# Kernel tuning notes

Measured on AMD Instinct MI355X. Metric: run time of the kernel, lower is better.

Reference implementation:

```python
import jax, jax.numpy as jnp
import numpy as np

T = 35            # cfg.VOXEL_POINT_COUNT
D, H, W = 10, 400, 352  # cfg.INPUT_DEPTH/HEIGHT/WIDTH
EPS = 1e-5


def _vfe(x, mask, w, b, gamma, beta):
    # x: [K, T, Cin]; mask: [K, T, 1]
    h = jax.nn.relu(jnp.einsum('ktc,cu->ktu', x, w) + b)        # [K, T, U]
    mean = jnp.mean(h, axis=(0, 1))
    var = jnp.var(h, axis=(0, 1))
    h = (h - mean) * jax.lax.rsqrt(var + EPS) * gamma + beta    # batch-stat BN
    agg = jnp.max(h, axis=1, keepdims=True)                     # [K, 1, U]
    cat = jnp.concatenate([h, jnp.broadcast_to(agg, h.shape)], axis=-1)  # [K, T, 2U]
    return cat * mask


def setup_inputs() -> dict:
    key = jax.random.key(0)
    ks = jax.random.split(key, 12)
    K = 40000
    feature = jax.random.normal(ks[0], (K, T, 7), dtype=jnp.float32)
    # zero out ~half the points so the nonzero mask is meaningful
    keep = jax.random.bernoulli(ks[1], 0.5, (K, T, 1)).astype(jnp.float32)
    feature = feature * keep
    bidx = jax.random.randint(ks[2], (K, 1), 0, 2)
    didx = jax.random.randint(ks[3], (K, 1), 0, D)
    hidx = jax.random.randint(ks[4], (K, 1), 0, H)
    widx = jax.random.randint(ks[5], (K, 1), 0, W)
    coordinate = jnp.concatenate([bidx, didx, hidx, widx], axis=1).astype(jnp.int32)
    s = 0.1
    return {
        'feature': feature,
        'w1': jax.random.normal(ks[6], (7, 16), dtype=jnp.float32) * s,
        'b1': jnp.zeros((16,), dtype=jnp.float32),
        'gamma1': jnp.ones((16,), dtype=jnp.float32),
        'beta1': jnp.zeros((16,), dtype=jnp.float32),
        'w2': jax.random.normal(ks[7], (32, 32), dtype=jnp.float32) * s,
        'b2': jnp.zeros((32,), dtype=jnp.float32),
        'gamma2': jnp.ones((32,), dtype=jnp.float32),
        'beta2': jnp.zeros((32,), dtype=jnp.float32),
        'coordinate': coordinate,
        'batch_size': 2,
    }


def reference(feature, w1, b1, gamma1, beta1, w2, b2, gamma2, beta2, coordinate, batch_size):
    # mask: voxel point is valid if any channel nonzero (max over channels != 0)
    mask = (jnp.max(feature, axis=2, keepdims=True) != 0).astype(feature.dtype)  # [K, T, 1]
    x = _vfe(feature, mask, w1, b1, gamma1, beta1)   # [K, T, 32]
    x = _vfe(x, mask, w2, b2, gamma2, beta2)         # [K, T, 64]
    voxelwise = jnp.max(x, axis=1)                   # [K, 64]
    out = jnp.zeros((batch_size, D, H, W, 64), dtype=voxelwise.dtype)
    out = out.at[coordinate[:, 0], coordinate[:, 1], coordinate[:, 2], coordinate[:, 3]].add(voxelwise)
    return out
```

## Files before the change

kernel.cpp:

```cpp
#include <hip/hip_runtime.h>
#include <math.h>

#define TT 35
#define DD 10
#define HD 400
#define WD 352
#define CIN 7
#define U1 16
#define U2 32
#define EPSV 1e-5f

#define WS_SUM1 256
#define WS_SSQ1 768
#define WS_SUM2 1280
#define WS_SSQ2 1792
#define NC1 32
#define NC2 16
#define WS_ZERO_FLOATS 2304
#define WS_SUM_OFF 4096

typedef __bf16 bf16x8 __attribute__((ext_vector_type(8)));
typedef float f32x4 __attribute__((ext_vector_type(4)));

__device__ inline unsigned short f2bf(float x) {
  unsigned u = __builtin_bit_cast(unsigned, x);
  unsigned r = (u + 0x7fff + ((u >> 16) & 1)) >> 16;
  return (unsigned short)r;
}

__global__ __launch_bounds__(256) void k_stats1(
    const float* __restrict__ feat, const float* __restrict__ w1,
    const float* __restrict__ b1, float* __restrict__ ws, int P) {
  __shared__ float s_w1[CIN * U1];
  __shared__ float s_b1[U1];
  __shared__ float s_red[4][2 * U1];

  int tid = threadIdx.x;
  if (tid < CIN * U1) s_w1[tid] = w1[tid];
  if (tid < U1) s_b1[tid] = b1[tid];
  __syncthreads();

  float sum[U1], ssq[U1];
#pragma unroll
  for (int u = 0; u < U1; ++u) { sum[u] = 0.f; ssq[u] = 0.f; }

  int stride = gridDim.x * blockDim.x;
  for (int p = blockIdx.x * blockDim.x + tid; p < P; p += stride) {
    const float* f = feat + (size_t)p * CIN;
    float x[CIN];
#pragma unroll
    for (int c = 0; c < CIN; ++c) x[c] = f[c];
#pragma unroll
    for (int u = 0; u < U1; ++u) {
      float acc = s_b1[u];
#pragma unroll
      for (int c = 0; c < CIN; ++c) acc += x[c] * s_w1[c * U1 + u];
      float h = fmaxf(acc, 0.f);
      sum[u] += h;
      ssq[u] += h * h;
    }
  }

  int lane = tid & 63, wv = tid >> 6;
#pragma unroll
  for (int u = 0; u < U1; ++u) {
    float s = sum[u], q = ssq[u];
    for (int off = 32; off; off >>= 1) {
      s += __shfl_down(s, off);
      q += __shfl_down(q, off);
    }
    if (lane == 0) { s_red[wv][u] = s; s_red[wv][U1 + u] = q; }
  }
  __syncthreads();
  if (tid < 2 * U1) {
    float tot = s_red[0][tid] + s_red[1][tid] + s_red[2][tid] + s_red[3][tid];
    int copy = blockIdx.x & (NC1 - 1);
    int u = tid & (U1 - 1);
    int base = (tid < U1) ? WS_SUM1 : WS_SSQ1;
    atomicAdd(&ws[base + copy * U1 + u], tot);
  }
}

__global__ __launch_bounds__(256) void k_vfe2(
    const float* __restrict__ feat, const float* __restrict__ w1,
    const float* __restrict__ b1, const float* __restrict__ g1,
    const float* __restrict__ be1, const float* __restrict__ w2,
    const float* __restrict__ b2, float* __restrict__ ws,
    float* __restrict__ sumg, float* __restrict__ cntg, int K, float invN) {
  __shared__ unsigned short s_w2b[32 * 40];
  __shared__ unsigned short s_catb[4][48][32];
  __shared__ float s_mk[4][40];
  __shared__ float s_red[4][64];

  int tid = threadIdx.x;
  int lane = tid & 63, wv = tid >> 6;
  int g = lane >> 4, u = lane & 15;
  int v = blockIdx.x * 4 + wv;
  bool active = (v < K);

  for (int i = tid; i < 32 * 32; i += 256) {
    int n = i >> 5, cp = i & 31;
    int c = (cp & 1) ? (16 + (cp >> 1)) : (cp >> 1);
    s_w2b[n * 40 + cp] = f2bf(w2[c * 32 + n]);
  }
  {
    unsigned* z = (unsigned*)s_catb;
    for (int i = tid; i < 4 * 13 * 16; i += 256) {
      int w = i / 208, rem = i % 208;
      int row = 35 + (rem >> 4), k = rem & 15;
      z[(w * 48 + row) * 16 + k] = 0u;
    }
  }

  float s1 = 0.f, q1 = 0.f;
#pragma unroll
  for (int c = 0; c < NC1; ++c) {
    s1 += ws[WS_SUM1 + c * U1 + u];
    q1 += ws[WS_SSQ1 + c * U1 + u];
  }
  float mean1 = s1 * invN;
  float var1 = q1 * invN - mean1 * mean1;
  float A1 = g1[u] / sqrtf(var1 + EPSV);
  float B1 = be1[u] - mean1 * A1;

  float w1r[CIN];
#pragma unroll
  for (int c = 0; c < CIN; ++c) w1r[c] = w1[c * U1 + u];
  float b1u = b1[u];

  float h1n[9], mkv[9];
  float aggl = -INFINITY;
  float cntl = 0.f;
  const float* fv = feat + (size_t)v * (TT * CIN);
#pragma unroll
  for (int j = 0; j < 9; ++j) {
    int t = g + 4 * j;
    h1n[j] = -INFINITY;
    mkv[j] = 0.f;
    if (active && t < TT) {
      const float* fr = fv + t * CIN;
      float x0 = fr[0], x1 = fr[1], x2 = fr[2], x3 = fr[3];
      float x4 = fr[4], x5 = fr[5], x6 = fr[6];
      float m = fmaxf(fmaxf(fmaxf(x0, x1), fmaxf(x2, x3)),
                      fmaxf(fmaxf(x4, x5), x6));
      float mk = (m != 0.f) ? 1.f : 0.f;
      float acc = b1u + x0 * w1r[0] + x1 * w1r[1] + x2 * w1r[2] +
                  x3 * w1r[3] + x4 * w1r[4] + x5 * w1r[5] + x6 * w1r[6];
      float h = fmaxf(acc, 0.f);
      h1n[j] = A1 * h + B1;
      mkv[j] = mk;
      cntl += mk;
      if (u == 0) s_mk[wv][t] = mk;
      aggl = fmaxf(aggl, h1n[j]);
    }
  }
  aggl = fmaxf(aggl, __shfl_xor(aggl, 16));
  aggl = fmaxf(aggl, __shfl_xor(aggl, 32));
  cntl += __shfl_xor(cntl, 16);
  cntl += __shfl_xor(cntl, 32);
  if (active && lane == 0) cntg[v] = cntl;

#pragma unroll
  for (int j = 0; j < 9; ++j) {
    int t = g + 4 * j;
    if (active && t < TT) {
      unsigned pk = (unsigned)f2bf(h1n[j] * mkv[j]) |
                    ((unsigned)f2bf(aggl * mkv[j]) << 16);
      *(unsigned*)&s_catb[wv][t][2 * u] = pk;
    }
  }
  __syncthreads();

  f32x4 acc[2][3];
#pragma unroll
  for (int nt = 0; nt < 2; ++nt)
#pragma unroll
    for (int mt = 0; mt < 3; ++mt) acc[nt][mt] = (f32x4)(0.f);

  bf16x8 bfr[2];
#pragma unroll
  for (int nt = 0; nt < 2; ++nt) {
    uint4 raw = *(const uint4*)&s_w2b[(nt * 16 + u) * 40 + g * 8];
    bfr[nt] = __builtin_bit_cast(bf16x8, raw);
  }
#pragma unroll
  for (int mt = 0; mt < 3; ++mt) {
    uint4 raw = *(const uint4*)&s_catb[wv][mt * 16 + u][g * 8];
    bf16x8 afr = __builtin_bit_cast(bf16x8, raw);
#pragma unroll
    for (int nt = 0; nt < 2; ++nt)
      acc[nt][mt] =
          __builtin_amdgcn_mfma_f32_16x16x32_bf16(afr, bfr[nt], acc[nt][mt], 0, 0, 0);
  }

  float b2c[2] = {b2[u], b2[16 + u]};
  float sum[2] = {0.f, 0.f}, ssq[2] = {0.f, 0.f};
  float maxm[2] = {-INFINITY, -INFINITY}, minm[2] = {INFINITY, INFINITY};
  float maxa[2] = {-INFINITY, -INFINITY}, mina[2] = {INFINITY, INFINITY};
#pragma unroll
  for (int nt = 0; nt < 2; ++nt) {
#pragma unroll
    for (int mt = 0; mt < 3; ++mt) {
#pragma unroll
      for (int r = 0; r < 4; ++r) {
        int row = mt * 16 + g * 4 + r;
        if (row < TT) {
          float h = fmaxf(acc[nt][mt][r] + b2c[nt], 0.f);
          sum[nt] += h;
          ssq[nt] += h * h;
          maxa[nt] = fmaxf(maxa[nt], h);
          mina[nt] = fminf(mina[nt], h);
          float mk = s_mk[wv][row];
          if (mk != 0.f) {
            maxm[nt] = fmaxf(maxm[nt], h);
            minm[nt] = fminf(minm[nt], h);
          }
        }
      }
    }
  }

#pragma unroll
  for (int nt = 0; nt < 2; ++nt) {
    sum[nt] += __shfl_xor(sum[nt], 16);
    sum[nt] += __shfl_xor(sum[nt], 32);
    ssq[nt] += __shfl_xor(ssq[nt], 16);
    ssq[nt] += __shfl_xor(ssq[nt], 32);
    maxa[nt] = fmaxf(maxa[nt], __shfl_xor(maxa[nt], 16));
    maxa[nt] = fmaxf(maxa[nt], __shfl_xor(maxa[nt], 32));
    mina[nt] = fminf(mina[nt], __shfl_xor(mina[nt], 16));
    mina[nt] = fminf(mina[nt], __shfl_xor(mina[nt], 32));
    maxm[nt] = fmaxf(maxm[nt], __shfl_xor(maxm[nt], 16));
    maxm[nt] = fmaxf(maxm[nt], __shfl_xor(maxm[nt], 32));
    minm[nt] = fminf(minm[nt], __shfl_xor(minm[nt], 16));
    minm[nt] = fminf(minm[nt], __shfl_xor(minm[nt], 32));
  }
  if (active && g == 0) {
#pragma unroll
    for (int nt = 0; nt < 2; ++nt) {
      float4 sm = make_float4(maxm[nt], minm[nt], maxa[nt], mina[nt]);
      *(float4*)&sumg[(size_t)v * 128 + (nt * 16 + u) * 4] = sm;
    }
  }

  float contrib = 0.f;
  if (active) {
    contrib = (g == 0) ? sum[0] : (g == 1) ? sum[1] : (g == 2) ? ssq[0] : ssq[1];
  }
  s_red[wv][(g & 1) * 16 + u + (g >> 1) * 32] = contrib;
  __syncthreads();
  if (tid < 64) {
    float tot = s_red[0][tid] + s_red[1][tid] + s_red[2][tid] + s_red[3][tid];
    int copy = blockIdx.x & (NC2 - 1);
    int ch = tid & 31;
    int base = (tid < 32) ? WS_SUM2 : WS_SSQ2;
    atomicAdd(&ws[base + copy * U2 + ch], tot);
  }
}

__global__ __launch_bounds__(256) void k_final(
    const float* __restrict__ sumg, const float* __restrict__ cntg,
    const float* __restrict__ ws, const float* __restrict__ g2,
    const float* __restrict__ be2, const int* __restrict__ coord,
    float* __restrict__ out, int K, float invN) {
  int tid = threadIdx.x;
  int v = blockIdx.x * 8 + (tid >> 5);
  int ch = tid & 31;
  if (v >= K) return;

  float s = 0.f, q = 0.f;
#pragma unroll
  for (int c = 0; c < NC2; ++c) {
    s += ws[WS_SUM2 + c * U2 + ch];
    q += ws[WS_SSQ2 + c * U2 + ch];
  }
  float mean = s * invN;
  float var = q * invN - mean * mean;
  float A2 = g2[ch] / sqrtf(var + EPSV);
  float B2 = be2[ch] - mean * A2;

  float4 sm = *(const float4*)&sumg[(size_t)v * 128 + ch * 4];
  float cnt = cntg[v];

  float hm = (A2 >= 0.f) ? (A2 * sm.x + B2) : (A2 * sm.y + B2);
  float ag = (A2 >= 0.f) ? (A2 * sm.z + B2) : (A2 * sm.w + B2);
  float voxr = (cnt < 0.5f) ? 0.f : ((cnt > TT - 0.5f) ? hm : fmaxf(hm, 0.f));
  float voxa = (cnt < 0.5f) ? 0.f : ((cnt > TT - 0.5f) ? ag : fmaxf(ag, 0.f));

  const int4 cd = *(const int4*)&coord[4 * v];
  long base = ((((long)cd.x * DD + cd.y) * HD + cd.z) * WD + cd.w) * 64;
  atomicAdd(&out[base + ch], voxr);
  atomicAdd(&out[base + 32 + ch], voxa);
}

extern "C" void kernel_launch(void* const* d_in, const int* in_sizes, int n_in,
                              void* d_out, int out_size, void* d_ws,
                              size_t ws_size, hipStream_t stream) {
  const float* feat = (const float*)d_in[0];
  const float* w1 = (const float*)d_in[1];
  const float* b1 = (const float*)d_in[2];
  const float* g1 = (const float*)d_in[3];
  const float* be1 = (const float*)d_in[4];
  const float* w2 = (const float*)d_in[5];
  const float* b2 = (const float*)d_in[6];
  const float* g2 = (const float*)d_in[7];
  const float* be2 = (const float*)d_in[8];
  const int* coord = (const int*)d_in[9];
  float* out = (float*)d_out;
  float* ws = (float*)d_ws;

  int K = in_sizes[0] / (TT * CIN);
  int P = K * TT;
  float invN = 1.0f / (float)P;

  float* sumg = ws + WS_SUM_OFF;
  float* cntg = sumg + (size_t)K * 128;

  (void)hipMemsetAsync(d_out, 0, (size_t)out_size * sizeof(float), stream);
  (void)hipMemsetAsync(d_ws, 0, WS_ZERO_FLOATS * sizeof(float), stream);

  k_stats1<<<512, 256, 0, stream>>>(feat, w1, b1, ws, P);

  int vb = (K + 3) / 4;
  k_vfe2<<<vb, 256, 0, stream>>>(feat, w1, b1, g1, be1, w2, b2, ws, sumg, cntg,
                                 K, invN);
  k_final<<<(K + 7) / 8, 256, 0, stream>>>(sumg, cntg, ws, g2, be2, coord, out,
                                           K, invN);
}
```

Baseline: 834.2 us.

## Loop k_vfe2 blocks over voxel groups and compute BN coefficients once per block

k_vfe2 now runs a grid-stride loop in which each block handles four groups of four voxels. The bf16 W2 staging, zero padding, layer-1 BN statistics reduction and weight register loads are therefore done once per block and reused across groups. The layer-1 and layer-2 BN scale/shift reductions are computed once per block in shared memory, instead of every thread reading all the partial-sum copies. k_final gets the same treatment, and k_stats1 launches four times as many blocks. This trims redundant global reads and setup work, at the cost of fewer k_vfe2 blocks and an extra barrier per loop iteration. The large output memset and the scatter atomics are untouched.

```diff
diff --git a/kernel.cpp b/kernel.cpp
--- a/kernel.cpp
+++ b/kernel.cpp
@@ -86,17 +86,17 @@
     const float* __restrict__ b1, const float* __restrict__ g1,
     const float* __restrict__ be1, const float* __restrict__ w2,
     const float* __restrict__ b2, float* __restrict__ ws,
-    float* __restrict__ sumg, float* __restrict__ cntg, int K, float invN) {
+    float* __restrict__ sumg, float* __restrict__ cntg, int K, float invN,
+    int G) {
   __shared__ unsigned short s_w2b[32 * 40];
   __shared__ unsigned short s_catb[4][48][32];
   __shared__ float s_mk[4][40];
   __shared__ float s_red[4][64];
+  __shared__ float s_A1[U1], s_B1[U1];
 
   int tid = threadIdx.x;
   int lane = tid & 63, wv = tid >> 6;
   int g = lane >> 4, u = lane & 15;
-  int v = blockIdx.x * 4 + wv;
-  bool active = (v < K);
 
   for (int i = tid; i < 32 * 32; i += 256) {
     int n = i >> 5, cp = i & 31;
@@ -111,150 +111,162 @@
       z[(w * 48 + row) * 16 + k] = 0u;
     }
   }
-
-  float s1 = 0.f, q1 = 0.f;
-#pragma unroll
-  for (int c = 0; c < NC1; ++c) {
-    s1 += ws[WS_SUM1 + c * U1 + u];
-    q1 += ws[WS_SSQ1 + c * U1 + u];
-  }
-  float mean1 = s1 * invN;
-  float var1 = q1 * invN - mean1 * mean1;
-  float A1 = g1[u] / sqrtf(var1 + EPSV);
-  float B1 = be1[u] - mean1 * A1;
-
+  if (tid < 32) {
+    int ch = tid & 15;
+    int base = (tid < 16) ? WS_SUM1 : WS_SSQ1;
+    float acc = 0.f;
+#pragma unroll
+    for (int c = 0; c < NC1; ++c) acc += ws[base + c * U1 + ch];
+    s_red[0][tid] = acc;
+  }
+  __syncthreads();
+  if (tid < 16) {
+    float s = s_red[0][tid], q = s_red[0][16 + tid];
+    float mean = s * invN;
+    float var = q * invN - mean * mean;
+    float A = g1[tid] / sqrtf(var + EPSV);
+    s_A1[tid] = A;
+    s_B1[tid] = be1[tid] - mean * A;
+  }
+  __syncthreads();
+
+  float A1 = s_A1[u], B1 = s_B1[u];
   float w1r[CIN];
 #pragma unroll
   for (int c = 0; c < CIN; ++c) w1r[c] = w1[c * U1 + u];
   float b1u = b1[u];
-
-  float h1n[9], mkv[9];
-  float aggl = -INFINITY;
-  float cntl = 0.f;
-  const float* fv = feat + (size_t)v * (TT * CIN);
-#pragma unroll
-  for (int j = 0; j < 9; ++j) {
-    int t = g + 4 * j;
-    h1n[j] = -INFINITY;
-    mkv[j] = 0.f;
-    if (active && t < TT) {
-      const float* fr = fv + t * CIN;
-      float x0 = fr[0], x1 = fr[1], x2 = fr[2], x3 = fr[3];
-      float x4 = fr[4], x5 = fr[5], x6 = fr[6];
-      float m = fmaxf(fmaxf(fmaxf(x0, x1), fmaxf(x2, x3)),
-                      fmaxf(fmaxf(x4, x5), x6));
-      float mk = (m != 0.f) ? 1.f : 0.f;
-      float acc = b1u + x0 * w1r[0] + x1 * w1r[1] + x2 * w1r[2] +
-                  x3 * w1r[3] + x4 * w1r[4] + x5 * w1r[5] + x6 * w1r[6];
-      float h = fmaxf(acc, 0.f);
-      h1n[j] = A1 * h + B1;
-      mkv[j] = mk;
-      cntl += mk;
-      if (u == 0) s_mk[wv][t] = mk;
-      aggl = fmaxf(aggl, h1n[j]);
-    }
-  }
-  aggl = fmaxf(aggl, __shfl_xor(aggl, 16));
-  aggl = fmaxf(aggl, __shfl_xor(aggl, 32));
-  cntl += __shfl_xor(cntl, 16);
-  cntl += __shfl_xor(cntl, 32);
-  if (active && lane == 0) cntg[v] = cntl;
-
-#pragma unroll
-  for (int j = 0; j < 9; ++j) {
-    int t = g + 4 * j;
-    if (active && t < TT) {
-      unsigned pk = (unsigned)f2bf(h1n[j] * mkv[j]) |
-                    ((unsigned)f2bf(aggl * mkv[j]) << 16);
-      *(unsigned*)&s_catb[wv][t][2 * u] = pk;
-    }
-  }
-  __syncthreads();
-
-  f32x4 acc[2][3];
-#pragma unroll
-  for (int nt = 0; nt < 2; ++nt)
-#pragma unroll
-    for (int mt = 0; mt < 3; ++mt) acc[nt][mt] = (f32x4)(0.f);
-
+  float b2c[2] = {b2[u], b2[16 + u]};
   bf16x8 bfr[2];
 #pragma unroll
   for (int nt = 0; nt < 2; ++nt) {
     uint4 raw = *(const uint4*)&s_w2b[(nt * 16 + u) * 40 + g * 8];
     bfr[nt] = __builtin_bit_cast(bf16x8, raw);
   }
-#pragma unroll
-  for (int mt = 0; mt < 3; ++mt) {
-    uint4 raw = *(const uint4*)&s_catb[wv][mt * 16 + u][g * 8];
-    bf16x8 afr = __builtin_bit_cast(bf16x8, raw);
+
+  for (int grp = blockIdx.x; grp < G; grp += gridDim.x) {
+    __syncthreads();
+    int v = grp * 4 + wv;
+    bool active = (v < K);
+
+    float h1n[9], mkv[9];
+    float aggl = -INFINITY;
+    float cntl = 0.f;
+    const float* fv = feat + (size_t)v * (TT * CIN);
+#pragma unroll
+    for (int j = 0; j < 9; ++j) {
+      int t = g + 4 * j;
+      h1n[j] = -INFINITY;
+      mkv[j] = 0.f;
+      if (active && t < TT) {
+        const float* fr = fv + t * CIN;
+        float x0 = fr[0], x1 = fr[1], x2 = fr[2], x3 = fr[3];
+        float x4 = fr[4], x5 = fr[5], x6 = fr[6];
+        float m = fmaxf(fmaxf(fmaxf(x0, x1), fmaxf(x2, x3)),
+                        fmaxf(fmaxf(x4, x5), x6));
+        float mk = (m != 0.f) ? 1.f : 0.f;
+        float acc = b1u + x0 * w1r[0] + x1 * w1r[1] + x2 * w1r[2] +
+                    x3 * w1r[3] + x4 * w1r[4] + x5 * w1r[5] + x6 * w1r[6];
+        float h = fmaxf(acc, 0.f);
+        h1n[j] = A1 * h + B1;
+        mkv[j] = mk;
+        cntl += mk;
+        if (u == 0) s_mk[wv][t] = mk;
+        aggl = fmaxf(aggl, h1n[j]);
+      }
+    }
+    aggl = fmaxf(aggl, __shfl_xor(aggl, 16));
+    aggl = fmaxf(aggl, __shfl_xor(aggl, 32));
+    cntl += __shfl_xor(cntl, 16);
+    cntl += __shfl_xor(cntl, 32);
+    if (active && lane == 0) cntg[v] = cntl;
+
+#pragma unroll
+    for (int j = 0; j < 9; ++j) {
+      int t = g + 4 * j;
+      if (active && t < TT) {
+        unsigned pk = (unsigned)f2bf(h1n[j] * mkv[j]) |
+                      ((unsigned)f2bf(aggl * mkv[j]) << 16);
+        *(unsigned*)&s_catb[wv][t][2 * u] = pk;
+      }
+    }
+
+    f32x4 acc[2][3];
 #pragma unroll
     for (int nt = 0; nt < 2; ++nt)
-      acc[nt][mt] =
-          __builtin_amdgcn_mfma_f32_16x16x32_bf16(afr, bfr[nt], acc[nt][mt], 0, 0, 0);
-  }
-
-  float b2c[2] = {b2[u], b2[16 + u]};
-  float sum[2] = {0.f, 0.f}, ssq[2] = {0.f, 0.f};
-  float maxm[2] = {-INFINITY, -INFINITY}, minm[2] = {INFINITY, INFINITY};
-  float maxa[2] = {-INFINITY, -INFINITY}, mina[2] = {INFINITY, INFINITY};
-#pragma unroll
-  for (int nt = 0; nt < 2; ++nt) {
+#pragma unroll
+      for (int mt = 0; mt < 3; ++mt) acc[nt][mt] = (f32x4)(0.f);
 #pragma unroll
     for (int mt = 0; mt < 3; ++mt) {
-#pragma unroll
-      for (int r = 0; r < 4; ++r) {
-        int row = mt * 16 + g * 4 + r;
-        if (row < TT) {
-          float h = fmaxf(acc[nt][mt][r] + b2c[nt], 0.f);
-          sum[nt] += h;
-          ssq[nt] += h * h;
-          maxa[nt] = fmaxf(maxa[nt], h);
-          mina[nt] = fminf(mina[nt], h);
-          float mk = s_mk[wv][row];
-          if (mk != 0.f) {
-            maxm[nt] = fmaxf(maxm[nt], h);
-            minm[nt] = fminf(minm[nt], h);
+      uint4 raw = *(const uint4*)&s_catb[wv][mt * 16 + u][g * 8];
+      bf16x8 afr = __builtin_bit_cast(bf16x8, raw);
+#pragma unroll
+      for (int nt = 0; nt < 2; ++nt)
+        acc[nt][mt] = __builtin_amdgcn_mfma_f32_16x16x32_bf16(afr, bfr[nt],
+                                                              acc[nt][mt], 0, 0, 0);
+    }
+
+    float sum[2] = {0.f, 0.f}, ssq[2] = {0.f, 0.f};
+    float maxm[2] = {-INFINITY, -INFINITY}, minm[2] = {INFINITY, INFINITY};
+    float maxa[2] = {-INFINITY, -INFINITY}, mina[2] = {INFINITY, INFINITY};
+#pragma unroll
+    for (int nt = 0; nt < 2; ++nt) {
+#pragma unroll
+      for (int mt = 0; mt < 3; ++mt) {
+#pragma unroll
+        for (int r = 0; r < 4; ++r) {
+          int row = mt * 16 + g * 4 + r;
+          if (row < TT) {
+            float h = fmaxf(acc[nt][mt][r] + b2c[nt], 0.f);
+            sum[nt] += h;
+            ssq[nt] += h * h;
+            maxa[nt] = fmaxf(maxa[nt], h);
+            mina[nt] = fminf(mina[nt], h);
+            float mk = s_mk[wv][row];
+            if (mk != 0.f) {
+              maxm[nt] = fmaxf(maxm[nt], h);
+              minm[nt] = fminf(minm[nt], h);
+            }
           }
         }
       }
     }
-  }
-
-#pragma unroll
-  for (int nt = 0; nt < 2; ++nt) {
-    sum[nt] += __shfl_xor(sum[nt], 16);
-    sum[nt] += __shfl_xor(sum[nt], 32);
-    ssq[nt] += __shfl_xor(ssq[nt], 16);
-    ssq[nt] += __shfl_xor(ssq[nt], 32);
-    maxa[nt] = fmaxf(maxa[nt], __shfl_xor(maxa[nt], 16));
-    maxa[nt] = fmaxf(maxa[nt], __shfl_xor(maxa[nt], 32));
-    mina[nt] = fminf(mina[nt], __shfl_xor(mina[nt], 16));
-    mina[nt] = fminf(mina[nt], __shfl_xor(mina[nt], 32));
-    maxm[nt] = fmaxf(maxm[nt], __shfl_xor(maxm[nt], 16));
-    maxm[nt] = fmaxf(maxm[nt], __shfl_xor(maxm[nt], 32));
-    minm[nt] = fminf(minm[nt], __shfl_xor(minm[nt], 16));
-    minm[nt] = fminf(minm[nt], __shfl_xor(minm[nt], 32));
-  }
-  if (active && g == 0) {
+
 #pragma unroll
     for (int nt = 0; nt < 2; ++nt) {
-      float4 sm = make_float4(maxm[nt], minm[nt], maxa[nt], mina[nt]);
-      *(float4*)&sumg[(size_t)v * 128 + (nt * 16 + u) * 4] = sm;
-    }
-  }
-
-  float contrib = 0.f;
-  if (active) {
-    contrib = (g == 0) ? sum[0] : (g == 1) ? sum[1] : (g == 2) ? ssq[0] : ssq[1];
-  }
-  s_red[wv][(g & 1) * 16 + u + (g >> 1) * 32] = contrib;
-  __syncthreads();
-  if (tid < 64) {
-    float tot = s_red[0][tid] + s_red[1][tid] + s_red[2][tid] + s_red[3][tid];
-    int copy = blockIdx.x & (NC2 - 1);
-    int ch = tid & 31;
-    int base = (tid < 32) ? WS_SUM2 : WS_SSQ2;
-    atomicAdd(&ws[base + copy * U2 + ch], tot);
+      sum[nt] += __shfl_xor(sum[nt], 16);
+      sum[nt] += __shfl_xor(sum[nt], 32);
+      ssq[nt] += __shfl_xor(ssq[nt], 16);
+      ssq[nt] += __shfl_xor(ssq[nt], 32);
+      maxa[nt] = fmaxf(maxa[nt], __shfl_xor(maxa[nt], 16));
+      maxa[nt] = fmaxf(maxa[nt], __shfl_xor(maxa[nt], 32));
+      mina[nt] = fminf(mina[nt], __shfl_xor(mina[nt], 16));
+      mina[nt] = fminf(mina[nt], __shfl_xor(mina[nt], 32));
+      maxm[nt] = fmaxf(maxm[nt], __shfl_xor(maxm[nt], 16));
+      maxm[nt] = fmaxf(maxm[nt], __shfl_xor(maxm[nt], 32));
+      minm[nt] = fminf(minm[nt], __shfl_xor(minm[nt], 16));
+      minm[nt] = fminf(minm[nt], __shfl_xor(minm[nt], 32));
+    }
+    if (active && g == 0) {
+#pragma unroll
+      for (int nt = 0; nt < 2; ++nt) {
+        float4 sm = make_float4(maxm[nt], minm[nt], maxa[nt], mina[nt]);
+        *(float4*)&sumg[(size_t)v * 128 + (nt * 16 + u) * 4] = sm;
+      }
+    }
+
+    float contrib = 0.f;
+    if (active) {
+      contrib = (g == 0) ? sum[0] : (g == 1) ? sum[1] : (g == 2) ? ssq[0] : ssq[1];
+    }
+    s_red[wv][(g & 1) * 16 + u + (g >> 1) * 32] = contrib;
+    __syncthreads();
+    if (tid < 64) {
+      float tot = s_red[0][tid] + s_red[1][tid] + s_red[2][tid] + s_red[3][tid];
+      int copy = blockIdx.x & (NC2 - 1);
+      int ch = tid & 31;
+      int base = (tid < 32) ? WS_SUM2 : WS_SSQ2;
+      atomicAdd(&ws[base + copy * U2 + ch], tot);
+    }
   }
 }
 
@@ -263,34 +275,45 @@
     const float* __restrict__ ws, const float* __restrict__ g2,
     const float* __restrict__ be2, const int* __restrict__ coord,
     float* __restrict__ out, int K, float invN) {
+  __shared__ float s_tmp[64];
+  __shared__ float s_A2[U2], s_B2[U2];
   int tid = threadIdx.x;
+
+  if (tid < 64) {
+    int ch = tid & 31;
+    int base = (tid < 32) ? WS_SUM2 : WS_SSQ2;
+    float acc = 0.f;
+#pragma unroll
+    for (int c = 0; c < NC2; ++c) acc += ws[base + c * U2 + ch];
+    s_tmp[tid] = acc;
+  }
+  __syncthreads();
+  if (tid < 32) {
+    float mean = s_tmp[tid] * invN;
+    float var = s_tmp[32 + tid] * invN - mean * mean;
+    float A = g2[tid] / sqrtf(var + EPSV);
+    s_A2[tid] = A;
+    s_B2[tid] = be2[tid] - mean * A;
+  }
+  __syncthreads();
+
   int v = blockIdx.x * 8 + (tid >> 5);
   int ch = tid & 31;
-  if (v >= K) return;
-
-  float s = 0.f, q = 0.f;
-#pragma unroll
-  for (int c = 0; c < NC2; ++c) {
-    s += ws[WS_SUM2 + c * U2 + ch];
-    q += ws[WS_SSQ2 + c * U2 + ch];
-  }
-  float mean = s * invN;
-  float var = q * invN - mean * mean;
-  float A2 = g2[ch] / sqrtf(var + EPSV);
-  float B2 = be2[ch] - mean * A2;
-
-  float4 sm = *(const float4*)&sumg[(size_t)v * 128 + ch * 4];
-  float cnt = cntg[v];
-
-  float hm = (A2 >= 0.f) ? (A2 * sm.x + B2) : (A2 * sm.y + B2);
-  float ag = (A2 >= 0.f) ? (A2 * sm.z + B2) : (A2 * sm.w + B2);
-  float voxr = (cnt < 0.5f) ? 0.f : ((cnt > TT - 0.5f) ? hm : fmaxf(hm, 0.f));
-  float voxa = (cnt < 0.5f) ? 0.f : ((cnt > TT - 0.5f) ? ag : fmaxf(ag, 0.f));
-
-  const int4 cd = *(const int4*)&coord[4 * v];
-  long base = ((((long)cd.x * DD + cd.y) * HD + cd.z) * WD + cd.w) * 64;
-  atomicAdd(&out[base + ch], voxr);
-  atomicAdd(&out[base + 32 + ch], voxa);
+  if (v < K) {
+    float A2 = s_A2[ch], B2 = s_B2[ch];
+    float4 sm = *(const float4*)&sumg[(size_t)v * 128 + ch * 4];
+    float cnt = cntg[v];
+
+    float hm = (A2 >= 0.f) ? (A2 * sm.x + B2) : (A2 * sm.y + B2);
+    float ag = (A2 >= 0.f) ? (A2 * sm.z + B2) : (A2 * sm.w + B2);
+    float voxr = (cnt < 0.5f) ? 0.f : ((cnt > TT - 0.5f) ? hm : fmaxf(hm, 0.f));
+    float voxa = (cnt < 0.5f) ? 0.f : ((cnt > TT - 0.5f) ? ag : fmaxf(ag, 0.f));
+
+    const int4 cd = *(const int4*)&coord[4 * v];
+    long base = ((((long)cd.x * DD + cd.y) * HD + cd.z) * WD + cd.w) * 64;
+    atomicAdd(&out[base + ch], voxr);
+    atomicAdd(&out[base + 32 + ch], voxa);
+  }
 }
 
 extern "C" void kernel_launch(void* const* d_in, const int* in_sizes, int n_in,
@@ -319,11 +342,12 @@
   (void)hipMemsetAsync(d_out, 0, (size_t)out_size * sizeof(float), stream);
   (void)hipMemsetAsync(d_ws, 0, WS_ZERO_FLOATS * sizeof(float), stream);
 
-  k_stats1<<<512, 256, 0, stream>>>(feat, w1, b1, ws, P);
-
-  int vb = (K + 3) / 4;
+  k_stats1<<<2048, 256, 0, stream>>>(feat, w1, b1, ws, P);
+
+  int G = (K + 3) / 4;
+  int vb = (G + 3) / 4;
   k_vfe2<<<vb, 256, 0, stream>>>(feat, w1, b1, g1, be1, w2, b2, ws, sumg, cntg,
-                                 K, invN);
+                                 K, invN, G);
   k_final<<<(K + 7) / 8, 256, 0, stream>>>(sumg, cntg, ws, g2, be2, coord, out,
                                            K, invN);
 }
```

Result: no change. 842.2 us, median of 2 (+1.0%).
